# Optimization experiments

Hardware: AMD Instinct MI355X
Metric: run time of the kernel (lower is better)

## Reference

```python
import jax, jax.numpy as jnp
import numpy as np

WS = 7          # window_size
DIM = 256
H = 8           # num_heads
HD = DIM // H   # head_dim = 32
NW = 64         # windows per image
B = 64          # batch of images
B_ = B * NW
M_ = WS * WS + 1  # 50 tokens (cls + patches)


def _relative_position_index():
    coords = np.stack(np.meshgrid(np.arange(WS), np.arange(WS), indexing='ij'))  # (2, ws, ws)
    flat = coords.reshape(2, -1)  # (2, ws*ws)
    rel = flat[:, :, None] - flat[:, None, :]  # (2, N, N)
    rel = rel.transpose(1, 2, 0).astype(np.int64)
    rel[:, :, 0] += WS - 1
    rel[:, :, 1] += WS - 1
    rel[:, :, 0] *= 2 * WS - 1
    return rel.sum(-1).astype(np.int32)  # (N, N) in [0, (2ws-1)^2)


def setup_inputs() -> dict:
    key = jax.random.key(0)
    k1, k2, k3 = jax.random.split(key, 3)
    qkv = jax.random.normal(k1, (B_, M_, 3 * DIM), dtype=jnp.float32)
    mask = jax.random.normal(k2, (NW, M_ - 1, M_), dtype=jnp.float32)
    bias_table = jax.random.normal(k3, ((2 * WS - 1) ** 2, H), dtype=jnp.float32) * 0.02
    rel_index = jnp.asarray(_relative_position_index())
    return {"qkv": qkv, "mask": mask, "bias_table": bias_table, "rel_index": rel_index}


def reference(qkv, mask, bias_table, rel_index):
    Bw, M, C = qkv.shape
    scale = HD ** -0.5
    # (3, B_, H, M, hd)
    qkv = qkv.reshape(Bw, M, 3, H, HD).transpose(2, 0, 3, 1, 4)
    q = qkv[0][:, :, 1:, :] * scale   # queries drop cls token: (B_, H, M-1, hd)
    k, v = qkv[1], qkv[2]             # (B_, H, M, hd)
    attn = jnp.einsum('bhqd,bhkd->bhqk', q, k)  # (B_, H, M-1, M)
    # relative position bias over patch-patch block only
    N = WS * WS
    bias = bias_table[rel_index.reshape(-1)].reshape(N, N, H).transpose(2, 0, 1)  # (H, N, N)
    attn = jnp.concatenate([attn[..., :1], attn[..., 1:] + bias[None]], axis=-1)
    # additive window mask
    nW = mask.shape[0]
    attn = attn.reshape(Bw // nW, nW, H, M - 1, M) + mask[None, :, None]
    attn = jax.nn.softmax(attn.reshape(Bw, H, M - 1, M), axis=-1)
    x = jnp.einsum('bhqk,bhkd->bqhd', attn, v).reshape(Bw, M - 1, DIM)
    return x
```

## Files before the change

### kernel.cpp

```cpp
#include <hip/hip_runtime.h>
#include <stdint.h>

#define NQ 49
#define MT 50
#define NH 8
#define HD 32
#define NW 64
#define BWIN 4096

typedef __attribute__((ext_vector_type(8))) short short8;
typedef __attribute__((ext_vector_type(4))) float f32x4;
typedef __attribute__((ext_vector_type(4))) uint32_t u32x4;

__device__ __forceinline__ uint32_t f2u(float x){ union{float f;uint32_t u;}c; c.f=x; return c.u; }
__device__ __forceinline__ float u2f(uint32_t u){ union{float f;uint32_t u;}c; c.u=u; return c.f; }
__device__ __forceinline__ uint32_t bf16rn(float x){
  uint32_t u = f2u(x);
  return (u + 0x7fffu + ((u >> 16) & 1u)) >> 16;
}
__device__ __forceinline__ void bsplit(float x, uint32_t& hi, uint32_t& lo){
  hi = bf16rn(x);
  float hf = u2f(hi << 16);
  lo = bf16rn(x - hf);
}

__global__ __launch_bounds__(64, 2)
void winattn_kernel(const float* __restrict__ qkv,
                    const float* __restrict__ mask,
                    const float* __restrict__ bias_table,
                    const int*   __restrict__ rel_index,
                    float* __restrict__ out)
{
  __shared__ uint32_t sP[64 * 68];

  const int id   = blockIdx.x;
  const int b    = id >> 3;
  const int h    = id & 7;
  const int w    = b & (NW - 1);
  const int lane = threadIdx.x;
  const int ln   = lane & 15;
  const int qd   = lane >> 4;

  const float* base = qkv + (size_t)b * (MT * 3 * 256);

  short8 qh[4], ql[4], kh[4], kl[4];
  const float scale = 0.17677669529663687f;

#pragma unroll
  for (int t = 0; t < 4; ++t) {
    int m   = 16 * t + ln;
    int tok = (m < NQ ? m : NQ - 1) + 1;
    const float* p = base + (size_t)tok * 768 + h * HD + qd * 8;
    f32x4 e0 = *(const f32x4*)p;
    f32x4 e1 = *(const f32x4*)(p + 4);
#pragma unroll
    for (int j = 0; j < 8; ++j) {
      float x = (j < 4 ? e0[j] : e1[j - 4]) * scale;
      uint32_t hi, lo; bsplit(x, hi, lo);
      qh[t][j] = (short)(unsigned short)hi;
      ql[t][j] = (short)(unsigned short)lo;
    }
  }
#pragma unroll
  for (int u = 0; u < 4; ++u) {
    int n    = 16 * u + ln;
    int ktok = (n < MT ? n : MT - 1);
    const float* p = base + (size_t)ktok * 768 + 256 + h * HD + qd * 8;
    f32x4 e0 = *(const f32x4*)p;
    f32x4 e1 = *(const f32x4*)(p + 4);
#pragma unroll
    for (int j = 0; j < 8; ++j) {
      float x = (j < 4 ? e0[j] : e1[j - 4]);
      uint32_t hi, lo; bsplit(x, hi, lo);
      kh[u][j] = (short)(unsigned short)hi;
      kl[u][j] = (short)(unsigned short)lo;
    }
  }

  f32x4 S[4][4];
#pragma unroll
  for (int t = 0; t < 4; ++t) {
#pragma unroll
    for (int u = 0; u < 4; ++u) {
      f32x4 a = {0.f, 0.f, 0.f, 0.f};
      a = __builtin_amdgcn_mfma_f32_16x16x32_bf16(qh[t], kh[u], a, 0, 0, 0);
      a = __builtin_amdgcn_mfma_f32_16x16x32_bf16(qh[t], kl[u], a, 0, 0, 0);
      a = __builtin_amdgcn_mfma_f32_16x16x32_bf16(ql[t], kh[u], a, 0, 0, 0);
      S[t][u] = a;
    }
  }

#pragma unroll
  for (int t = 0; t < 4; ++t) {
#pragma unroll
    for (int r = 0; r < 4; ++r) {
      int i = 16 * t + 4 * qd + r;
#pragma unroll
      for (int u = 0; u < 4; ++u) {
        int j = 16 * u + ln;
        if (j >= MT) {
          S[t][u][r] = -1e30f;
        } else if (i < NQ) {
          float am = mask[(w * NQ + i) * MT + j];
          if (j > 0) {
            int idx = rel_index[i * NQ + (j - 1)];
            am += bias_table[idx * NH + h];
          }
          S[t][u][r] += am;
        }
      }
    }
  }

  float rsumv[4][4];
#pragma unroll
  for (int t = 0; t < 4; ++t) {
#pragma unroll
    for (int r = 0; r < 4; ++r) {
      float mx = fmaxf(fmaxf(S[t][0][r], S[t][1][r]), fmaxf(S[t][2][r], S[t][3][r]));
#pragma unroll
      for (int s = 1; s < 16; s <<= 1) mx = fmaxf(mx, __shfl_xor(mx, s, 16));
      int row = 16 * t + 4 * qd + r;
      float sum = 0.f;
#pragma unroll
      for (int u = 0; u < 4; ++u) {
        float p = exp2f((S[t][u][r] - mx) * 1.4426950408889634f);
        sum += p;
        uint32_t hi, lo; bsplit(p, hi, lo);
        sP[row * 68 + 16 * u + ln] = (hi << 16) | lo;
      }
#pragma unroll
      for (int s = 1; s < 16; s <<= 1) sum += __shfl_xor(sum, s, 16);
      rsumv[t][r] = sum;
    }
  }
  __syncthreads();

  short8 vh[2][2], vl[2][2];
#pragma unroll
  for (int kt = 0; kt < 2; ++kt) {
#pragma unroll
    for (int u2 = 0; u2 < 2; ++u2) {
#pragma unroll
      for (int j = 0; j < 8; ++j) {
        int k  = 32 * kt + 8 * qd + j;
        int d  = 16 * u2 + ln;
        int kc = (k < MT ? k : MT - 1);
        float x = base[(size_t)kc * 768 + 512 + h * HD + d];
        if (k >= MT) x = 0.f;
        uint32_t hi, lo; bsplit(x, hi, lo);
        vh[kt][u2][j] = (short)(unsigned short)hi;
        vl[kt][u2][j] = (short)(unsigned short)lo;
      }
    }
  }

  f32x4 O[4][2];
#pragma unroll
  for (int t = 0; t < 4; ++t)
#pragma unroll
    for (int u2 = 0; u2 < 2; ++u2) O[t][u2] = (f32x4){0.f, 0.f, 0.f, 0.f};

#pragma unroll
  for (int kt = 0; kt < 2; ++kt) {
#pragma unroll
    for (int t = 0; t < 4; ++t) {
      const uint32_t* pp = &sP[(16 * t + ln) * 68 + 32 * kt + 8 * qd];
      u32x4 w0 = *(const u32x4*)pp;
      u32x4 w1 = *(const u32x4*)(pp + 4);
      short8 ph, pl;
#pragma unroll
      for (int j = 0; j < 8; ++j) {
        uint32_t wv = (j < 4 ? w0[j] : w1[j - 4]);
        ph[j] = (short)(unsigned short)(wv >> 16);
        pl[j] = (short)(unsigned short)(wv & 0xffffu);
      }
#pragma unroll
      for (int u2 = 0; u2 < 2; ++u2) {
        f32x4 a = O[t][u2];
        a = __builtin_amdgcn_mfma_f32_16x16x32_bf16(ph, vh[kt][u2], a, 0, 0, 0);
        a = __builtin_amdgcn_mfma_f32_16x16x32_bf16(pl, vh[kt][u2], a, 0, 0, 0);
        a = __builtin_amdgcn_mfma_f32_16x16x32_bf16(ph, vl[kt][u2], a, 0, 0, 0);
        O[t][u2] = a;
      }
    }
  }

#pragma unroll
  for (int t = 0; t < 4; ++t) {
#pragma unroll
    for (int r = 0; r < 4; ++r) {
      int row = 16 * t + 4 * qd + r;
      if (row >= NQ) continue;
      float inv = 1.0f / rsumv[t][r];
#pragma unroll
      for (int u2 = 0; u2 < 2; ++u2) {
        int d = 16 * u2 + ln;
        out[(((size_t)b * NQ + row) * NH + h) * HD + d] = O[t][u2][r] * inv;
      }
    }
  }
}

extern "C" void kernel_launch(void* const* d_in, const int* in_sizes, int n_in,
                              void* d_out, int out_size, void* d_ws, size_t ws_size,
                              hipStream_t stream) {
  (void)in_sizes; (void)n_in; (void)d_ws; (void)ws_size; (void)out_size;
  const float* qkv        = (const float*)d_in[0];
  const float* mask       = (const float*)d_in[1];
  const float* bias_table = (const float*)d_in[2];
  const int*   rel_index  = (const int*)d_in[3];
  float* out = (float*)d_out;

  dim3 grid(BWIN * NH);
  winattn_kernel<<<grid, 64, 0, stream>>>(qkv, mask, bias_table, rel_index, out);
}
```

Measured before the change: 1.175 ms.

## Precompute mask+bias table, drop P low half, swizzle LDS, two heads per block

Adds a prologue kernel that folds the window mask and gathered relative-position bias into one per-(window,head) table in workspace, so the attention kernel does one load per score instead of three dependent gathers. Softmax probabilities are now stored as a single bf16 in a XOR-swizzled LDS layout and read back with one vector load. This removes one of the three MFMAs in P·V, at the cost of some accuracy in P. Blocks now hold two waves covering two heads of the same window, and the launch bounds change accordingly.

```diff
diff --git a/kernel.cpp b/kernel.cpp
--- a/kernel.cpp
+++ b/kernel.cpp
@@ -7,10 +7,10 @@
 #define HD 32
 #define NW 64
 #define BWIN 4096
+#define M2TOT (NW*NH*NQ*MT)
 
 typedef __attribute__((ext_vector_type(8))) short short8;
 typedef __attribute__((ext_vector_type(4))) float f32x4;
-typedef __attribute__((ext_vector_type(4))) uint32_t u32x4;
 
 __device__ __forceinline__ uint32_t f2u(float x){ union{float f;uint32_t u;}c; c.f=x; return c.u; }
 __device__ __forceinline__ float u2f(uint32_t u){ union{float f;uint32_t u;}c; c.u=u; return c.f; }
@@ -20,32 +20,48 @@
 }
 __device__ __forceinline__ void bsplit(float x, uint32_t& hi, uint32_t& lo){
   hi = bf16rn(x);
-  float hf = u2f(hi << 16);
-  lo = bf16rn(x - hf);
-}
-
-__global__ __launch_bounds__(64, 2)
+  lo = bf16rn(x - u2f(hi << 16));
+}
+
+__global__ void fuse_mb(const float* __restrict__ mask,
+                        const float* __restrict__ bias_table,
+                        const int*   __restrict__ rel_index,
+                        float* __restrict__ M2)
+{
+  int idx = blockIdx.x * 256 + threadIdx.x;
+  if (idx >= M2TOT) return;
+  int j  = idx % MT;
+  int t  = idx / MT;
+  int i  = t % NQ;
+  int t2 = t / NQ;
+  int h  = t2 % NH;
+  int w  = t2 / NH;
+  float v = mask[(w * NQ + i) * MT + j];
+  if (j > 0) v += bias_table[rel_index[i * NQ + (j - 1)] * NH + h];
+  M2[idx] = v;
+}
+
+__global__ __launch_bounds__(128, 4)
 void winattn_kernel(const float* __restrict__ qkv,
-                    const float* __restrict__ mask,
-                    const float* __restrict__ bias_table,
-                    const int*   __restrict__ rel_index,
+                    const float* __restrict__ M2,
                     float* __restrict__ out)
 {
-  __shared__ uint32_t sP[64 * 68];
-
-  const int id   = blockIdx.x;
-  const int b    = id >> 3;
-  const int h    = id & 7;
-  const int w    = b & (NW - 1);
-  const int lane = threadIdx.x;
+  __shared__ unsigned short sP[2][64 * 64];
+
+  const int wv   = threadIdx.x >> 6;
+  const int lane = threadIdx.x & 63;
   const int ln   = lane & 15;
   const int qd   = lane >> 4;
 
+  const int id = blockIdx.x;
+  const int b  = id >> 2;
+  const int h  = ((id & 3) << 1) | wv;
+  const int w  = b & (NW - 1);
+
   const float* base = qkv + (size_t)b * (MT * 3 * 256);
+  const float scale = 0.17677669529663687f;
 
   short8 qh[4], ql[4], kh[4], kl[4];
-  const float scale = 0.17677669529663687f;
-
 #pragma unroll
   for (int t = 0; t < 4; ++t) {
     int m   = 16 * t + ln;
@@ -90,6 +106,7 @@
     }
   }
 
+  const float* mrow = M2 + ((size_t)(w * NH + h) * NQ) * MT;
 #pragma unroll
   for (int t = 0; t < 4; ++t) {
 #pragma unroll
@@ -98,16 +115,8 @@
 #pragma unroll
       for (int u = 0; u < 4; ++u) {
         int j = 16 * u + ln;
-        if (j >= MT) {
-          S[t][u][r] = -1e30f;
-        } else if (i < NQ) {
-          float am = mask[(w * NQ + i) * MT + j];
-          if (j > 0) {
-            int idx = rel_index[i * NQ + (j - 1)];
-            am += bias_table[idx * NH + h];
-          }
-          S[t][u][r] += am;
-        }
+        if (j >= MT)      S[t][u][r] = -1e30f;
+        else if (i < NQ)  S[t][u][r] += mrow[i * MT + j];
       }
     }
   }
@@ -120,14 +129,16 @@
       float mx = fmaxf(fmaxf(S[t][0][r], S[t][1][r]), fmaxf(S[t][2][r], S[t][3][r]));
 #pragma unroll
       for (int s = 1; s < 16; s <<= 1) mx = fmaxf(mx, __shfl_xor(mx, s, 16));
-      int row = 16 * t + 4 * qd + r;
+      int m  = 16 * t + 4 * qd + r;
+      int m7 = m & 7;
       float sum = 0.f;
 #pragma unroll
       for (int u = 0; u < 4; ++u) {
         float p = exp2f((S[t][u][r] - mx) * 1.4426950408889634f);
         sum += p;
-        uint32_t hi, lo; bsplit(p, hi, lo);
-        sP[row * 68 + 16 * u + ln] = (hi << 16) | lo;
+        int c = 16 * u + ln;
+        int addr = m * 64 + ((((c >> 3) ^ m7) << 3) | (c & 7));
+        sP[wv][addr] = (unsigned short)bf16rn(p);
       }
 #pragma unroll
       for (int s = 1; s < 16; s <<= 1) sum += __shfl_xor(sum, s, 16);
@@ -165,21 +176,13 @@
   for (int kt = 0; kt < 2; ++kt) {
 #pragma unroll
     for (int t = 0; t < 4; ++t) {
-      const uint32_t* pp = &sP[(16 * t + ln) * 68 + 32 * kt + 8 * qd];
-      u32x4 w0 = *(const u32x4*)pp;
-      u32x4 w1 = *(const u32x4*)(pp + 4);
-      short8 ph, pl;
-#pragma unroll
-      for (int j = 0; j < 8; ++j) {
-        uint32_t wv = (j < 4 ? w0[j] : w1[j - 4]);
-        ph[j] = (short)(unsigned short)(wv >> 16);
-        pl[j] = (short)(unsigned short)(wv & 0xffffu);
-      }
+      int m = 16 * t + ln;
+      int phys = ((4 * kt + qd) ^ (ln & 7));
+      short8 ph = *(const short8*)&sP[wv][m * 64 + (phys << 3)];
 #pragma unroll
       for (int u2 = 0; u2 < 2; ++u2) {
         f32x4 a = O[t][u2];
         a = __builtin_amdgcn_mfma_f32_16x16x32_bf16(ph, vh[kt][u2], a, 0, 0, 0);
-        a = __builtin_amdgcn_mfma_f32_16x16x32_bf16(pl, vh[kt][u2], a, 0, 0, 0);
         a = __builtin_amdgcn_mfma_f32_16x16x32_bf16(ph, vl[kt][u2], a, 0, 0, 0);
         O[t][u2] = a;
       }
@@ -205,13 +208,14 @@
 extern "C" void kernel_launch(void* const* d_in, const int* in_sizes, int n_in,
                               void* d_out, int out_size, void* d_ws, size_t ws_size,
                               hipStream_t stream) {
-  (void)in_sizes; (void)n_in; (void)d_ws; (void)ws_size; (void)out_size;
+  (void)in_sizes; (void)n_in; (void)ws_size; (void)out_size;
   const float* qkv        = (const float*)d_in[0];
   const float* mask       = (const float*)d_in[1];
   const float* bias_table = (const float*)d_in[2];
   const int*   rel_index  = (const int*)d_in[3];
   float* out = (float*)d_out;
-
-  dim3 grid(BWIN * NH);
-  winattn_kernel<<<grid, 64, 0, stream>>>(qkv, mask, bias_table, rel_index, out);
-}
+  float* M2  = (float*)d_ws;
+
+  fuse_mb<<<(M2TOT + 255) / 256, 256, 0, stream>>>(mask, bias_table, rel_index, M2);
+  winattn_kernel<<<BWIN * 4, 128, 0, stream>>>(qkv, M2, out);
+}
```

Measured after the change: 944.7 us. 19.6% less time.
